# Performance work log

Measured on AMD Instinct MI355X. Metric: run time of the kernel, lower is better.

Reference implementation:

```python
import jax, jax.numpy as jnp
import numpy as np

KERNEL = 31  # median window size (librosa HPSS default)
POWER = 2.0
MARGIN = 1.0


def _median_last(x, k):
    # median filter along the last axis with zero padding ((k-1)//2 each side),
    # matching F.conv2d one-hot unfold + torch.median in the original.
    pad = (k - 1) // 2
    xp = jnp.pad(x, ((0, 0), (0, 0), (0, 0), (pad, pad)))
    W = x.shape[-1]
    # [B,C,H,W,k] sliding windows (k is a small fixed constant -> loop ok)
    windows = jnp.stack([xp[..., i:i + W] for i in range(k)], axis=-1)
    return jnp.median(windows, axis=-1)


def _median_freq(x, k):
    # median filter along the H (freq) axis
    pad = (k - 1) // 2
    xp = jnp.pad(x, ((0, 0), (0, 0), (pad, pad), (0, 0)))
    H = x.shape[-2]
    windows = jnp.stack([xp[..., i:i + H, :] for i in range(k)], axis=-1)
    return jnp.median(windows, axis=-1)


def _softmask(X, X_ref, power):
    tiny = jnp.finfo(X.dtype).tiny
    Z = jnp.maximum(X, X_ref)
    Z = jnp.where(Z < tiny, jnp.ones_like(Z), Z)
    m = (X / Z) ** power
    r = (X_ref / Z) ** power
    return m / (m + r)


def setup_inputs() -> dict:
    key = jax.random.key(0)
    S = jax.random.uniform(key, (2, 2, 1025, 1024), dtype=jnp.float32)
    return {"S": S}


def reference(S):
    # harmonic: median along time (kernel (1,31)); percussive: along freq (kernel (31,1))
    harm = _median_last(S, KERNEL)
    perc = _median_freq(S, KERNEL)
    mask_harm = _softmask(harm, perc * MARGIN, POWER)
    mask_perc = _softmask(perc, harm * MARGIN, POWER)
    return (S * mask_harm, S * mask_perc)
```

## Files before the change

kernel.cpp:

```cpp
#include <hip/hip_runtime.h>

#define BC 4
#define HD 1025
#define WD 1024
#define KWIN 31
#define CH 8

__device__ __forceinline__ void ce(float& x, float& y) {
    float lo = fminf(x, y);
    float hi = fmaxf(x, y);
    x = lo; y = hi;
}

__device__ __forceinline__ void sort31(float* a) {
#pragma unroll
    for (int pk = 4; pk >= 0; --pk) {
        const int p = 1 << pk;
#pragma unroll
        for (int k = 0; k <= 4 - pk; ++k) {
            const int d = (k == 0) ? p : ((16 >> (k - 1)) - p);
            const int r = (k == 0) ? 0 : p;
#pragma unroll
            for (int i = 0; i < KWIN - d; ++i)
                if ((i & p) == r) ce(a[i], a[i + d]);
        }
    }
}

__device__ __forceinline__ float slide_med(float* win, float oldv, float newv) {
    float r[KWIN - 1];
#pragma unroll
    for (int i = 0; i < KWIN - 1; ++i)
        r[i] = (win[i] >= oldv) ? win[i + 1] : win[i];
    win[0] = fminf(r[0], newv);
#pragma unroll
    for (int i = 1; i < KWIN - 1; ++i)
        win[i] = fmaxf(fminf(r[i], newv), r[i - 1]);
    win[KWIN - 1] = fmaxf(newv, r[KWIN - 2]);
    return win[15];
}

__device__ __forceinline__ float* swz(float* base, int f ) {
    int u = f >> 2;
    u ^= (u >> 3) & 7;
    return base + (u << 2);
}

__global__ __launch_bounds__(256, 4) void harm_kernel(const float* __restrict__ S,
                                                      float* __restrict__ harm) {
    __shared__ float lds[4 * 544];
    const int tid = threadIdx.x;
    const int wv = tid >> 6, ln = tid & 63;
    const int hr = blockIdx.x * 4 + wv;
    const int plane = blockIdx.z;
    const int row = hr >> 1, half = hr & 1;
    const bool rowok = (row < HD);
    float* wl = lds + wv * 544;
    const float* rowg = S + ((size_t)plane * HD + row) * WD;
    const int hw0 = half * 512;
    const int g0 = hw0 - 16;

    if (rowok) {
#pragma unroll
        for (int it = 0; it < 3; ++it) {
            int t = 4 * ln + 256 * it;
            if (t < 544) {
                int g = g0 + t;
                float4 v;
                if (g >= 0 && g + 3 < WD) {
                    v = *(const float4*)(rowg + g);
                } else {
                    v.x = ((unsigned)(g + 0) < WD) ? rowg[g + 0] : 0.f;
                    v.y = ((unsigned)(g + 1) < WD) ? rowg[g + 1] : 0.f;
                    v.z = ((unsigned)(g + 2) < WD) ? rowg[g + 2] : 0.f;
                    v.w = ((unsigned)(g + 3) < WD) ? rowg[g + 3] : 0.f;
                }
                *(float4*)swz(wl, t) = v;
            }
        }
    }
    __syncthreads();

    float med[CH];
    if (rowok) {
        float raw[40];
#pragma unroll
        for (int k = 0; k < 10; ++k) {
            float4 v = *(const float4*)swz(wl, 8 * ln + 4 * k);
            raw[4 * k + 0] = v.x; raw[4 * k + 1] = v.y;
            raw[4 * k + 2] = v.z; raw[4 * k + 3] = v.w;
        }
        float win[KWIN];
#pragma unroll
        for (int j = 0; j < KWIN; ++j) win[j] = raw[1 + j];
        sort31(win);
        med[0] = win[15];
#pragma unroll
        for (int s = 1; s < CH; ++s)
            med[s] = slide_med(win, raw[s] , raw[s + 31] );
    }
    __syncthreads();
    if (rowok) {
        *(float4*)swz(wl, 8 * ln)     = make_float4(med[0], med[1], med[2], med[3]);
        *(float4*)swz(wl, 8 * ln + 4) = make_float4(med[4], med[5], med[6], med[7]);
    }
    __syncthreads();
    if (rowok) {
        float* hrow = harm + ((size_t)plane * HD + row) * WD + hw0;
        float4 a = *(const float4*)swz(wl, 4 * ln);
        float4 b = *(const float4*)swz(wl, 256 + 4 * ln);
        *(float4*)(hrow + 4 * ln) = a;
        *(float4*)(hrow + 256 + 4 * ln) = b;
    }
}

__global__ __launch_bounds__(256, 4) void perc_mask_kernel(const float* __restrict__ S,
                                                           const float* __restrict__ harm,
                                                           float* __restrict__ out0,
                                                           float* __restrict__ out1) {
    const int w = blockIdx.x * 256 + threadIdx.x;
    const int h0 = blockIdx.y * CH;
    const int plane = blockIdx.z;
    const size_t poff = (size_t)plane * HD * WD;
    const float* base = S + poff;

    float span[38];
#pragma unroll
    for (int j = 0; j < 38; ++j) {
        int h = h0 - 15 + j;
        span[j] = ((unsigned)h < (unsigned)HD) ? base[(size_t)h * WD + w] : 0.f;
    }
    float hm[CH];
#pragma unroll
    for (int s = 0; s < CH; ++s) {
        int h = h0 + s;
        hm[s] = (h < HD) ? harm[poff + (size_t)h * WD + w] : 0.f;
    }

    float win[KWIN];
#pragma unroll
    for (int j = 0; j < KWIN; ++j) win[j] = span[j];
    sort31(win);

#pragma unroll
    for (int s = 0; s < CH; ++s) {
        int h = h0 + s;
        if (h >= HD) break;
        float pm = (s == 0) ? win[15] : slide_med(win, span[s - 1], span[s + 30]);
        float sv = span[15 + s];
        float h2 = hm[s] * hm[s];
        float p2 = pm * pm;
        float inv = 1.0f / (h2 + p2);
        size_t idx = poff + (size_t)h * WD + w;
        out0[idx] = sv * h2 * inv;
        out1[idx] = sv * p2 * inv;
    }
}

extern "C" void kernel_launch(void* const* d_in, const int* in_sizes, int n_in,
                              void* d_out, int out_size, void* d_ws, size_t ws_size,
                              hipStream_t stream) {
    const float* S = (const float*)d_in[0];
    float* out = (float*)d_out;
    const size_t N = (size_t)BC * HD * WD;
    float* harm = out;
    float* out1 = out + N;

    const int halfrows = HD * 2;
    dim3 hgrid((halfrows + 3) / 4, 1, BC);
    harm_kernel<<<hgrid, 256, 0, stream>>>(S, harm);

    dim3 pgrid(WD / 256, (HD + CH - 1) / CH, BC);
    perc_mask_kernel<<<pgrid, 256, 0, stream>>>(S, harm, out, out1);
}
```

Measured before the change: 100.7 us.

## Process full rows per wave in harm kernel, use fmed3 in sliding median

The harmonic kernel now gives each wave a full row, and each lane produces 16 outputs instead of 8. This amortizes the initial 31-element sort over more sliding steps and halves the redundant halo loads. Block-level __syncthreads are replaced with wave barriers because each wave only touches its own LDS region. The sliding-median update uses the fmed3 intrinsic so each step needs one instruction instead of a min/max pair. The percussive kernel now loads harm values lazily inside its loop. Per-lane register pressure in the harm kernel goes up.

```diff
diff --git a/kernel.cpp b/kernel.cpp
--- a/kernel.cpp
+++ b/kernel.cpp
@@ -4,7 +4,9 @@
 #define HD 1025
 #define WD 1024
 #define KWIN 31
-#define CH 8
+#define HCH 16
+#define PCH 8
+#define REG 1056
 
 __device__ __forceinline__ void ce(float& x, float& y) {
     float lo = fminf(x, y);
@@ -28,15 +30,15 @@
 }
 
 __device__ __forceinline__ float slide_med(float* win, float oldv, float newv) {
-    float r[KWIN - 1];
+    float rp = (win[0] >= oldv) ? win[1] : win[0];
+    win[0] = fminf(rp, newv);
 #pragma unroll
-    for (int i = 0; i < KWIN - 1; ++i)
-        r[i] = (win[i] >= oldv) ? win[i + 1] : win[i];
-    win[0] = fminf(r[0], newv);
-#pragma unroll
-    for (int i = 1; i < KWIN - 1; ++i)
-        win[i] = fmaxf(fminf(r[i], newv), r[i - 1]);
-    win[KWIN - 1] = fmaxf(newv, r[KWIN - 2]);
+    for (int i = 1; i < KWIN - 1; ++i) {
+        float rc = (win[i] >= oldv) ? win[i + 1] : win[i];
+        win[i] = __builtin_amdgcn_fmed3f(newv, rp, rc);
+        rp = rc;
+    }
+    win[KWIN - 1] = fmaxf(newv, rp);
     return win[15];
 }
 
@@ -48,24 +50,21 @@
 
 __global__ __launch_bounds__(256, 4) void harm_kernel(const float* __restrict__ S,
                                                       float* __restrict__ harm) {
-    __shared__ float lds[4 * 544];
+    __shared__ float lds[4 * REG];
     const int tid = threadIdx.x;
     const int wv = tid >> 6, ln = tid & 63;
-    const int hr = blockIdx.x * 4 + wv;
+    const int row = blockIdx.x * 4 + wv;
     const int plane = blockIdx.z;
-    const int row = hr >> 1, half = hr & 1;
     const bool rowok = (row < HD);
-    float* wl = lds + wv * 544;
+    float* wl = lds + wv * REG;
     const float* rowg = S + ((size_t)plane * HD + row) * WD;
-    const int hw0 = half * 512;
-    const int g0 = hw0 - 16;
 
     if (rowok) {
 #pragma unroll
-        for (int it = 0; it < 3; ++it) {
+        for (int it = 0; it < 5; ++it) {
             int t = 4 * ln + 256 * it;
-            if (t < 544) {
-                int g = g0 + t;
+            if (t < REG) {
+                int g = t - 16;
                 float4 v;
                 if (g >= 0 && g + 3 < WD) {
                     v = *(const float4*)(rowg + g);
@@ -79,14 +78,14 @@
             }
         }
     }
-    __syncthreads();
+    __builtin_amdgcn_wave_barrier();
 
-    float med[CH];
+    float m[HCH];
     if (rowok) {
-        float raw[40];
+        float raw[48];
 #pragma unroll
-        for (int k = 0; k < 10; ++k) {
-            float4 v = *(const float4*)swz(wl, 8 * ln + 4 * k);
+        for (int k = 0; k < 12; ++k) {
+            float4 v = *(const float4*)swz(wl, 16 * ln + 4 * k);
             raw[4 * k + 0] = v.x; raw[4 * k + 1] = v.y;
             raw[4 * k + 2] = v.z; raw[4 * k + 3] = v.w;
         }
@@ -94,23 +93,26 @@
 #pragma unroll
         for (int j = 0; j < KWIN; ++j) win[j] = raw[1 + j];
         sort31(win);
-        med[0] = win[15];
+        m[0] = win[15];
 #pragma unroll
-        for (int s = 1; s < CH; ++s)
-            med[s] = slide_med(win, raw[s] , raw[s + 31] );
+        for (int s = 1; s < HCH; ++s)
+            m[s] = slide_med(win, raw[s] , raw[s + 31] );
     }
-    __syncthreads();
+    __builtin_amdgcn_wave_barrier();
     if (rowok) {
-        *(float4*)swz(wl, 8 * ln)     = make_float4(med[0], med[1], med[2], med[3]);
-        *(float4*)swz(wl, 8 * ln + 4) = make_float4(med[4], med[5], med[6], med[7]);
+#pragma unroll
+        for (int g = 0; g < 4; ++g)
+            *(float4*)swz(wl, 16 * ln + 4 * g) =
+                make_float4(m[4 * g + 0], m[4 * g + 1], m[4 * g + 2], m[4 * g + 3]);
     }
-    __syncthreads();
+    __builtin_amdgcn_wave_barrier();
     if (rowok) {
-        float* hrow = harm + ((size_t)plane * HD + row) * WD + hw0;
-        float4 a = *(const float4*)swz(wl, 4 * ln);
-        float4 b = *(const float4*)swz(wl, 256 + 4 * ln);
-        *(float4*)(hrow + 4 * ln) = a;
-        *(float4*)(hrow + 256 + 4 * ln) = b;
+        float* hrow = harm + ((size_t)plane * HD + row) * WD;
+#pragma unroll
+        for (int it = 0; it < 4; ++it) {
+            int t = 4 * ln + 256 * it;
+            *(float4*)(hrow + t) = *(const float4*)swz(wl, t);
+        }
     }
 }
 
@@ -119,7 +121,7 @@
                                                            float* __restrict__ out0,
                                                            float* __restrict__ out1) {
     const int w = blockIdx.x * 256 + threadIdx.x;
-    const int h0 = blockIdx.y * CH;
+    const int h0 = blockIdx.y * PCH;
     const int plane = blockIdx.z;
     const size_t poff = (size_t)plane * HD * WD;
     const float* base = S + poff;
@@ -130,12 +132,6 @@
         int h = h0 - 15 + j;
         span[j] = ((unsigned)h < (unsigned)HD) ? base[(size_t)h * WD + w] : 0.f;
     }
-    float hm[CH];
-#pragma unroll
-    for (int s = 0; s < CH; ++s) {
-        int h = h0 + s;
-        hm[s] = (h < HD) ? harm[poff + (size_t)h * WD + w] : 0.f;
-    }
 
     float win[KWIN];
 #pragma unroll
@@ -143,15 +139,16 @@
     sort31(win);
 
 #pragma unroll
-    for (int s = 0; s < CH; ++s) {
+    for (int s = 0; s < PCH; ++s) {
         int h = h0 + s;
         if (h >= HD) break;
         float pm = (s == 0) ? win[15] : slide_med(win, span[s - 1], span[s + 30]);
         float sv = span[15 + s];
-        float h2 = hm[s] * hm[s];
+        size_t idx = poff + (size_t)h * WD + w;
+        float hmv = harm[idx];
+        float h2 = hmv * hmv;
         float p2 = pm * pm;
         float inv = 1.0f / (h2 + p2);
-        size_t idx = poff + (size_t)h * WD + w;
         out0[idx] = sv * h2 * inv;
         out1[idx] = sv * p2 * inv;
     }
@@ -166,10 +163,9 @@
     float* harm = out;
     float* out1 = out + N;
 
-    const int halfrows = HD * 2;
-    dim3 hgrid((halfrows + 3) / 4, 1, BC);
+    dim3 hgrid((HD + 3) / 4, 1, BC);
     harm_kernel<<<hgrid, 256, 0, stream>>>(S, harm);
 
-    dim3 pgrid(WD / 256, (HD + CH - 1) / CH, BC);
+    dim3 pgrid(WD / 256, (HD + PCH - 1) / PCH, BC);
     perc_mask_kernel<<<pgrid, 256, 0, stream>>>(S, harm, out, out1);
 }
```

Result: no change. 100.2 us (-0.5%).
